# Kernel optimization log

Measured on AMD Instinct MI355X. Metric: run time of the kernel, lower is better.

The kernel has to match this reference:

```python
import jax, jax.numpy as jnp
import numpy as np

B, SEQ, C_IN, D_MODEL = 64, 1534, 21, 516
M, TAU, KS, PAD, NK = 7, 3, 8, 21, 74  # kernel_size=m+1, pad=m*tau, num_kernels=74


def _sinusoid(n, d):
    # matches PositionalEmbedding / FixedEmbedding table construction
    pos = np.arange(n, dtype=np.float32)[:, None]
    div = np.exp(np.arange(0, d, 2, dtype=np.float32) * (-np.log(10000.0) / d))
    tab = np.zeros((n, d), dtype=np.float32)
    tab[:, 0::2] = np.sin(pos * div)
    tab[:, 1::2] = np.cos(pos * div)
    return jnp.asarray(tab)


def setup_inputs() -> dict:
    key = jax.random.key(0)
    k1, k2, k3 = jax.random.split(key, 3)
    x = jax.random.normal(k1, (B, SEQ, C_IN), dtype=jnp.float32)
    x_mark = jax.random.randint(k2, (B, SEQ, 5), 0, 4)
    kernels = jax.random.normal(k3, (NK, KS), dtype=jnp.float32)
    return {
        'x': x,
        'x_mark': x_mark,
        'kernels': kernels,
        'pe': _sinusoid(SEQ, D_MODEL),
        'hour_tab': _sinusoid(24, D_MODEL),
        'weekday_tab': _sinusoid(7, D_MODEL),
        'day_tab': _sinusoid(32, D_MODEL),
        'month_tab': _sinusoid(13, D_MODEL),
    }


def _token_embed(x, kernels):
    # Fuses the Python loop of 74 grouped conv1d launches into two einsums.
    b, L, c = x.shape
    xp = jnp.pad(x.transpose(0, 2, 1), ((0, 0), (0, 0), (PAD, 0)))  # [B,C,L+PAD]
    nw = (L + PAD - KS) // TAU + 1                                   # number of windows W
    idx = jnp.arange(nw)[:, None] * TAU + jnp.arange(KS)[None, :]    # [W,KS]
    win = xp[:, :, idx]                                              # [B,C,W,KS]
    # 73 depthwise kernels applied to every channel; concat order is kernel-major
    main = jnp.einsum('bcwk,nk->bwnc', win, kernels[:NK - 1]).reshape(b, nw, (NK - 1) * c)
    # last kernel applied to one randomly chosen channel (fixed to 0 for determinism)
    fin = jnp.einsum('bwk,k->bw', win[:, 0], kernels[NK - 1])[..., None]
    comb = jnp.concatenate([main, fin], axis=-1)                     # [B,W,73*C+1]
    return comb.transpose(0, 2, 1)[:, :, :L]                         # [B,73*C+1,W]


def reference(x, x_mark, kernels, pe, hour_tab, weekday_tab, day_tab, month_tab):
    L = x.shape[1]
    tok = _token_embed(x, kernels)                                   # [B, SEQ, D_MODEL]
    xm = x_mark.astype(jnp.int32)
    temp = (hour_tab[xm[:, :, 3]] + weekday_tab[xm[:, :, 2]]
            + day_tab[xm[:, :, 1]] + month_tab[xm[:, :, 0]])          # [B, SEQ, D_MODEL]
    # dropout in eval mode = identity
    return tok + pe[None, :L, :] + temp
```

## Files before the change

### kernel.cpp

```cpp
#include <hip/hip_runtime.h>

#define BATCH   64
#define SEQ     1534
#define C_IN    21
#define DM      516
#define NJ      129
#define KS      8
#define NK      74
#define PADL    21
#define NSPLIT  4

__global__ __launch_bounds__(256) void embed_kernel(
    const float* __restrict__ x,
    const int*   __restrict__ xm,
    const float* __restrict__ kernels,
    const float* __restrict__ pe,
    const float* __restrict__ hour_tab,
    const float* __restrict__ weekday_tab,
    const float* __restrict__ day_tab,
    const float* __restrict__ month_tab,
    float*       __restrict__ out)
{
    __shared__ float sk[NK * KS];
    for (int t = threadIdx.x; t < NK * KS; t += blockDim.x) sk[t] = kernels[t];
    __syncthreads();

    const int tid = blockIdx.x * blockDim.x + threadIdx.x;
    const int j     = tid % NJ;
    const int rest  = tid / NJ;
    const int s     = rest % NSPLIT;
    const int bc    = rest / NSPLIT;
    const int ch    = bc % C_IN;
    const int b     = bc / C_IN;

    float w[17];
    const int t0 = 12 * j - PADL;
#pragma unroll
    for (int u = 0; u < 17; ++u) {
        const int t = t0 + u;
        w[u] = (t >= 0 && t < SEQ) ? x[(b * SEQ + t) * C_IN + ch] : 0.0f;
    }

    const float4* pe4 = (const float4*)pe;
    const float4* h4  = (const float4*)hour_tab;
    const float4* wd4 = (const float4*)weekday_tab;
    const float4* dy4 = (const float4*)day_tab;
    const float4* mo4 = (const float4*)month_tab;
    float4*       o4  = (float4*)out;

    const int bSEQ = b * SEQ;

    for (int n = s; n < NK; n += NSPLIT) {
        if (n == NK - 1 && ch != 0) continue;
        const int i = n * C_IN + ch;

        float acc[4];
#pragma unroll
        for (int dd = 0; dd < 4; ++dd) {
            float a = 0.0f;
#pragma unroll
            for (int k = 0; k < KS; ++k) a += w[3 * dd + k] * sk[n * KS + k];
            acc[dd] = a;
        }

        const int* xr = xm + (bSEQ + i) * 5;
        const int hi = xr[3], wi = xr[2], di = xr[1], mi = xr[0];

        const float4 p  = pe4[i * NJ + j];
        const float4 th = h4 [hi * NJ + j];
        const float4 tw = wd4[wi * NJ + j];
        const float4 td = dy4[di * NJ + j];
        const float4 tm = mo4[mi * NJ + j];

        float4 o;
        o.x = acc[0] + p.x + th.x + tw.x + td.x + tm.x;
        o.y = acc[1] + p.y + th.y + tw.y + td.y + tm.y;
        o.z = acc[2] + p.z + th.z + tw.z + td.z + tm.z;
        o.w = acc[3] + p.w + th.w + tw.w + td.w + tm.w;

        o4[(bSEQ + i) * NJ + j] = o;
    }
}

extern "C" void kernel_launch(void* const* d_in, const int* in_sizes, int n_in,
                              void* d_out, int out_size, void* d_ws, size_t ws_size,
                              hipStream_t stream) {
    const float* x        = (const float*)d_in[0];
    const int*   x_mark   = (const int*)  d_in[1];
    const float* kernels  = (const float*)d_in[2];
    const float* pe       = (const float*)d_in[3];
    const float* hour_tab = (const float*)d_in[4];
    const float* wday_tab = (const float*)d_in[5];
    const float* day_tab  = (const float*)d_in[6];
    const float* mon_tab  = (const float*)d_in[7];
    float*       out      = (float*)d_out;

    const int total  = BATCH * C_IN * NSPLIT * NJ;
    const int blocks = (total + 255) / 256;
    embed_kernel<<<blocks, 256, 0, stream>>>(
        x, x_mark, kernels, pe, hour_tab, wday_tab, day_tab, mon_tab, out);
}
```

Before: 297.8 us.

## Stage input window in shared memory with per-block sequence tiling

Each block now owns one batch, one tile of 12 output columns and one kernel split. It cooperatively loads the padded x window for all channels into shared memory with contiguous reads. Threads are remapped as channel × column and read their 17-tap windows from LDS, replacing the strided per-thread global gathers. The tradeoff is that output stores for each row now form shorter contiguous runs of 12 float4s instead of full 129-column rows, and 4 of 256 threads sit idle.

```diff
diff --git a/kernel.cpp b/kernel.cpp
--- a/kernel.cpp
+++ b/kernel.cpp
@@ -9,6 +9,9 @@
 #define NK      74
 #define PADL    21
 #define NSPLIT  4
+#define JW      12
+#define NBJ     11
+#define TSPAN   (12*(JW-1) + 17)
 
 __global__ __launch_bounds__(256) void embed_kernel(
     const float* __restrict__ x,
@@ -22,24 +25,38 @@
     float*       __restrict__ out)
 {
     __shared__ float sk[NK * KS];
-    for (int t = threadIdx.x; t < NK * KS; t += blockDim.x) sk[t] = kernels[t];
+    __shared__ float sx[TSPAN * C_IN];
+
+    const int bid = blockIdx.x;
+    const int s   = bid % NSPLIT;
+    const int t1  = bid / NSPLIT;
+    const int jb  = t1 % NBJ;
+    const int b   = t1 / NBJ;
+    const int j0  = jb * JW;
+    const int t0  = 12 * j0 - PADL;
+
+    for (int t = threadIdx.x; t < NK * KS; t += 256) sk[t] = kernels[t];
+
+    {
+        const int base = (b * SEQ + t0) * C_IN;
+        const int lo   = -t0 * C_IN;
+        const int hi   = (SEQ - t0) * C_IN;
+        for (int p = threadIdx.x; p < TSPAN * C_IN; p += 256) {
+            float v = 0.0f;
+            if (p >= lo && p < hi) v = x[base + p];
+            sx[p] = v;
+        }
+    }
     __syncthreads();
 
-    const int tid = blockIdx.x * blockDim.x + threadIdx.x;
-    const int j     = tid % NJ;
-    const int rest  = tid / NJ;
-    const int s     = rest % NSPLIT;
-    const int bc    = rest / NSPLIT;
-    const int ch    = bc % C_IN;
-    const int b     = bc / C_IN;
+    const int ch = threadIdx.x / JW;
+    const int jj = threadIdx.x % JW;
+    const int j  = j0 + jj;
+    if (ch >= C_IN || j >= NJ) return;
 
     float w[17];
-    const int t0 = 12 * j - PADL;
 #pragma unroll
-    for (int u = 0; u < 17; ++u) {
-        const int t = t0 + u;
-        w[u] = (t >= 0 && t < SEQ) ? x[(b * SEQ + t) * C_IN + ch] : 0.0f;
-    }
+    for (int u = 0; u < 17; ++u) w[u] = sx[(12 * jj + u) * C_IN + ch];
 
     const float4* pe4 = (const float4*)pe;
     const float4* h4  = (const float4*)hour_tab;
@@ -95,8 +112,7 @@
     const float* mon_tab  = (const float*)d_in[7];
     float*       out      = (float*)d_out;
 
-    const int total  = BATCH * C_IN * NSPLIT * NJ;
-    const int blocks = (total + 255) / 256;
+    const int blocks = BATCH * NBJ * NSPLIT;
     embed_kernel<<<blocks, 256, 0, stream>>>(
         x, x_mark, kernels, pe, hour_tab, wday_tab, day_tab, mon_tab, out);
 }
```

Result: faster. 283.8 us (-4.7%).
